# Kernel tuning notes

Hardware: AMD Instinct MI355X
Metric: run time of the kernel (lower is better)

## Reference

```python
import jax, jax.numpy as jnp
import numpy as np

EPS = 1e-8  # torch F.cosine_similarity default eps


def setup_inputs() -> dict:
    key = jax.random.key(0)
    k1, k2 = jax.random.split(key)
    xs_pad = jax.random.normal(k1, (8, 8192, 256), dtype=jnp.float32)   # [B, T, D]
    spk_emb = jax.random.normal(k2, (8, 200, 256), dtype=jnp.float32)   # [B, S, D]
    return {"xs_pad": xs_pad, "spk_emb": spk_emb}


def reference(xs_pad, spk_emb):
    # Pairwise cosine similarity: [B, T, S]
    # Equivalent to F.cosine_similarity(xs.unsqueeze(2), spk.unsqueeze(1), dim=-1)
    # = dot(x, y) / max(||x|| * ||y||, eps)
    dot = jnp.einsum("btd,bsd->bts", xs_pad, spk_emb)
    nx = jnp.linalg.norm(xs_pad, axis=-1)    # [B, T]
    ny = jnp.linalg.norm(spk_emb, axis=-1)   # [B, S]
    denom = jnp.maximum(nx[:, :, None] * ny[:, None, :], EPS)
    return dot / denom
```

## Files before the change

kernel.cpp:

```cpp
#include <hip/hip_runtime.h>
#include <math.h>

typedef __attribute__((ext_vector_type(8))) _Float16 f16x8;
typedef __attribute__((ext_vector_type(4))) float f32x4;

#define BT 8192
#define BS 200
#define SP 208
#define DD 256
#define NJ 13
#define NKB 8

#define SLOT_H 512
#define PLANE_SLOTS (8 * NKB * NJ)
#define PLANE_H ((size_t)PLANE_SLOTS * SLOT_H)
#define WS_NEED (2 * PLANE_H * 2 + 8 * SP * 4)

__global__ __launch_bounds__(256, 4)
void spk_prep_kernel(const float* __restrict__ SPK, _Float16* __restrict__ wsH) {
    const int j = blockIdx.x;
    const int b = blockIdx.y;
    const int tid = threadIdx.x;
    const int w = tid >> 6;
    const int lane = tid & 63;
    const int lr = lane & 15;
    const int lg = lane >> 4;
    const int srow = j * 16 + lr;
    const float* __restrict__ spk_b = SPK + (size_t)b * BS * DD;

    __shared__ float pn[4][16];
    float ss = 0.f;

    #pragma unroll
    for (int t = 0; t < 2; ++t) {
        int kb = w + t * 4;
        f16x8 hi, lo;
        if (srow < BS) {
            const float* src = spk_b + srow * DD + kb * 32 + lg * 8;
            float4 v0 = *(const float4*)src;
            float4 v1 = *(const float4*)(src + 4);
            float xv[8] = {v0.x, v0.y, v0.z, v0.w, v1.x, v1.y, v1.z, v1.w};
            #pragma unroll
            for (int e = 0; e < 8; ++e) {
                _Float16 h = (_Float16)xv[e];
                hi[e] = h;
                lo[e] = (_Float16)(xv[e] - (float)h);
                ss = fmaf(xv[e], xv[e], ss);
            }
        } else {
            #pragma unroll
            for (int e = 0; e < 8; ++e) { hi[e] = (_Float16)0.f; lo[e] = (_Float16)0.f; }
        }
        size_t slot = ((size_t)(b * NKB + kb) * NJ + j) * SLOT_H + lane * 8;
        *(f16x8*)&wsH[slot] = hi;
        *(f16x8*)&wsH[PLANE_H + slot] = lo;
    }

    ss += __shfl_xor(ss, 16, 64);
    ss += __shfl_xor(ss, 32, 64);
    if (lane < 16) pn[w][lane] = ss;
    __syncthreads();
    if (tid < 16) {
        float s = pn[0][tid] + pn[1][tid] + pn[2][tid] + pn[3][tid];
        float* sn = (float*)(wsH + 2 * PLANE_H);
        sn[b * SP + j * 16 + tid] = sqrtf(s);
    }
}

__global__ __launch_bounds__(256, 4)
void cos_main_kernel(const float* __restrict__ X, const _Float16* __restrict__ wsH,
                     float* __restrict__ OUT) {
    const int b   = blockIdx.y;
    const int t0  = blockIdx.x * 64;
    const int tid = threadIdx.x;
    const int wid = tid >> 6;
    const int lane = tid & 63;
    const int lr = lane & 15;
    const int lg = lane >> 4;

    const float* __restrict__ xrow = X + ((size_t)b * BT + t0 + wid * 16 + lr) * DD;
    const float* __restrict__ snW = (const float*)(wsH + 2 * PLANE_H) + b * SP;

    float4 pa0 = *(const float4*)(xrow + lg * 8);
    float4 pa1 = *(const float4*)(xrow + lg * 8 + 4);

    f32x4 acc[NJ];
    #pragma unroll
    for (int j = 0; j < NJ; ++j) acc[j] = (f32x4){0.f, 0.f, 0.f, 0.f};
    float ss = 0.f;

    for (int kb = 0; kb < NKB; ++kb) {
        f16x8 ahi, alo;
        {
            float xv[8] = {pa0.x, pa0.y, pa0.z, pa0.w, pa1.x, pa1.y, pa1.z, pa1.w};
            #pragma unroll
            for (int e = 0; e < 8; ++e) {
                _Float16 h = (_Float16)xv[e];
                ahi[e] = h;
                alo[e] = (_Float16)(xv[e] - (float)h);
                ss = fmaf(xv[e], xv[e], ss);
            }
        }
        if (kb < NKB - 1) {
            int o = (kb + 1) * 32 + lg * 8;
            pa0 = *(const float4*)(xrow + o);
            pa1 = *(const float4*)(xrow + o + 4);
        }
        const _Float16* __restrict__ base =
            wsH + ((size_t)(b * NKB + kb) * NJ) * SLOT_H + lane * 8;
        #pragma unroll
        for (int j = 0; j < NJ; ++j) {
            f16x8 bhi = *(const f16x8*)(base + (size_t)j * SLOT_H);
            f16x8 blo = *(const f16x8*)(base + PLANE_H + (size_t)j * SLOT_H);
            acc[j] = __builtin_amdgcn_mfma_f32_16x16x32_f16(ahi, bhi, acc[j], 0, 0, 0);
            acc[j] = __builtin_amdgcn_mfma_f32_16x16x32_f16(alo, bhi, acc[j], 0, 0, 0);
            acc[j] = __builtin_amdgcn_mfma_f32_16x16x32_f16(ahi, blo, acc[j], 0, 0, 0);
        }
    }

    ss += __shfl_xor(ss, 16, 64);
    ss += __shfl_xor(ss, 32, 64);

    #pragma unroll
    for (int reg = 0; reg < 4; ++reg) {
        int rc = lg * 4 + reg;
        float xn = sqrtf(__shfl(ss, rc, 64));
        int row = t0 + wid * 16 + rc;
        float* orow = OUT + ((size_t)b * BT + row) * BS;
        #pragma unroll
        for (int j = 0; j < NJ; ++j) {
            int col = j * 16 + lr;
            if (col < BS) {
                float denom = fmaxf(xn * snW[col], 1e-8f);
                orow[col] = acc[j][reg] * __builtin_amdgcn_rcpf(denom);
            }
        }
    }
}

#define TM 128
#define LSTR 40

__global__ __launch_bounds__(256, 2)
void cos_scorer_kernel(const float* __restrict__ X, const float* __restrict__ SPK,
                       float* __restrict__ OUT) {
    const int b   = blockIdx.y;
    const int t0  = blockIdx.x * TM;
    const int tid = threadIdx.x;
    const int wid = tid >> 6;
    const int lane = tid & 63;
    const int lr  = lane & 15;
    const int lg  = lane >> 4;

    __shared__ _Float16 Shi[SP * LSTR];
    __shared__ _Float16 Slo[SP * LSTR];
    __shared__ float sn_l[SP];

    const float* __restrict__ spk_b = SPK + (size_t)b * BS * DD;
    const float* __restrict__ xrow0 = X + ((size_t)b * BT + t0 + wid * 32 + lr) * DD;
    const float* __restrict__ xrow1 = xrow0 + 16 * DD;

    float4 pa00 = *(const float4*)(xrow0 + lg * 8);
    float4 pa01 = *(const float4*)(xrow0 + lg * 8 + 4);
    float4 pa10 = *(const float4*)(xrow1 + lg * 8);
    float4 pa11 = *(const float4*)(xrow1 + lg * 8 + 4);

    if (tid < SP) {
        float ss = 0.f;
        if (tid < BS) {
            const float4* p = (const float4*)(spk_b + tid * DD);
            #pragma unroll 8
            for (int i = 0; i < DD / 4; ++i) {
                float4 v = p[i];
                ss = fmaf(v.x, v.x, ss); ss = fmaf(v.y, v.y, ss);
                ss = fmaf(v.z, v.z, ss); ss = fmaf(v.w, v.w, ss);
            }
        }
        sn_l[tid] = sqrtf(ss);
    }

    f32x4 acc[2][NJ];
    #pragma unroll
    for (int rt = 0; rt < 2; ++rt)
        #pragma unroll
        for (int j = 0; j < NJ; ++j)
            acc[rt][j] = (f32x4){0.f, 0.f, 0.f, 0.f};

    float ss0 = 0.f, ss1 = 0.f;

    for (int kb = 0; kb < 8; ++kb) {
        for (int i = tid; i < SP * 4; i += 256) {
            int s = i >> 2, part = i & 3;
            f16x8 hi, lo;
            #pragma unroll
            for (int e = 0; e < 8; ++e) { hi[e] = (_Float16)0.f; lo[e] = (_Float16)0.f; }
            if (s < BS) {
                const float* src = spk_b + s * DD + kb * 32 + part * 8;
                float4 v0 = *(const float4*)src;
                float4 v1 = *(const float4*)(src + 4);
                float xv[8] = {v0.x, v0.y, v0.z, v0.w, v1.x, v1.y, v1.z, v1.w};
                #pragma unroll
                for (int e = 0; e < 8; ++e) {
                    _Float16 h = (_Float16)xv[e];
                    hi[e] = h;
                    lo[e] = (_Float16)(xv[e] - (float)h);
                }
            }
            int off = s * LSTR + part * 8;
            *(f16x8*)&Shi[off] = hi;
            *(f16x8*)&Slo[off] = lo;
        }
        __syncthreads();

        f16x8 ahi0, alo0, ahi1, alo1;
        {
            float xv0[8] = {pa00.x, pa00.y, pa00.z, pa00.w, pa01.x, pa01.y, pa01.z, pa01.w};
            float xv1[8] = {pa10.x, pa10.y, pa10.z, pa10.w, pa11.x, pa11.y, pa11.z, pa11.w};
            #pragma unroll
            for (int e = 0; e < 8; ++e) {
                _Float16 h0 = (_Float16)xv0[e];
                ahi0[e] = h0; alo0[e] = (_Float16)(xv0[e] - (float)h0);
                ss0 = fmaf(xv0[e], xv0[e], ss0);
                _Float16 h1 = (_Float16)xv1[e];
                ahi1[e] = h1; alo1[e] = (_Float16)(xv1[e] - (float)h1);
                ss1 = fmaf(xv1[e], xv1[e], ss1);
            }
        }
        if (kb < 7) {
            int o = (kb + 1) * 32 + lg * 8;
            pa00 = *(const float4*)(xrow0 + o);
            pa01 = *(const float4*)(xrow0 + o + 4);
            pa10 = *(const float4*)(xrow1 + o);
            pa11 = *(const float4*)(xrow1 + o + 4);
        }

        #pragma unroll
        for (int j = 0; j < NJ; ++j) {
            int boff = (j * 16 + lr) * LSTR + lg * 8;
            f16x8 bhi = *(const f16x8*)&Shi[boff];
            f16x8 blo = *(const f16x8*)&Slo[boff];
            acc[0][j] = __builtin_amdgcn_mfma_f32_16x16x32_f16(ahi0, bhi, acc[0][j], 0, 0, 0);
            acc[1][j] = __builtin_amdgcn_mfma_f32_16x16x32_f16(ahi1, bhi, acc[1][j], 0, 0, 0);
            acc[0][j] = __builtin_amdgcn_mfma_f32_16x16x32_f16(alo0, bhi, acc[0][j], 0, 0, 0);
            acc[1][j] = __builtin_amdgcn_mfma_f32_16x16x32_f16(alo1, bhi, acc[1][j], 0, 0, 0);
            acc[0][j] = __builtin_amdgcn_mfma_f32_16x16x32_f16(ahi0, blo, acc[0][j], 0, 0, 0);
            acc[1][j] = __builtin_amdgcn_mfma_f32_16x16x32_f16(ahi1, blo, acc[1][j], 0, 0, 0);
        }
        __syncthreads();
    }

    ss0 += __shfl_xor(ss0, 16, 64);
    ss0 += __shfl_xor(ss0, 32, 64);
    ss1 += __shfl_xor(ss1, 16, 64);
    ss1 += __shfl_xor(ss1, 32, 64);

    #pragma unroll
    for (int rt = 0; rt < 2; ++rt) {
        float ssv = rt ? ss1 : ss0;
        #pragma unroll
        for (int reg = 0; reg < 4; ++reg) {
            int rc = lg * 4 + reg;
            float xn = sqrtf(__shfl(ssv, rc, 64));
            int row = t0 + wid * 32 + rt * 16 + rc;
            float* orow = OUT + ((size_t)b * BT + row) * BS;
            #pragma unroll
            for (int j = 0; j < NJ; ++j) {
                int col = j * 16 + lr;
                if (col < BS) {
                    float denom = fmaxf(xn * sn_l[col], 1e-8f);
                    orow[col] = acc[rt][j][reg] * __builtin_amdgcn_rcpf(denom);
                }
            }
        }
    }
}

extern "C" void kernel_launch(void* const* d_in, const int* in_sizes, int n_in,
                              void* d_out, int out_size, void* d_ws, size_t ws_size,
                              hipStream_t stream) {
    const float* X   = (const float*)d_in[0];
    const float* SPK = (const float*)d_in[1];
    float* OUT = (float*)d_out;

    if (ws_size >= (size_t)WS_NEED) {
        _Float16* wsH = (_Float16*)d_ws;
        hipLaunchKernelGGL(spk_prep_kernel, dim3(NJ, 8), dim3(256), 0, stream, SPK, wsH);
        hipLaunchKernelGGL(cos_main_kernel, dim3(BT / 64, 8), dim3(256), 0, stream,
                           X, wsH, OUT);
    } else {
        hipLaunchKernelGGL(cos_scorer_kernel, dim3(BT / TM, 8), dim3(256), 0, stream,
                           X, SPK, OUT);
    }
}
```

Before: 147.7 us.

## Stage speaker fragments in double-buffered LDS and give each wave two row tiles

The main kernel now copies the prepped fp16 hi/lo speaker fragments into a double-buffered shared-memory tile with direct global-to-LDS loads, prefetching the next k-block while the MFMAs run on the current one. Each wave handles two 16-row tiles instead of one, so every B fragment read from LDS feeds twice as many MFMAs. The workspace layout interleaves the hi and lo planes per k-block to make each copy contiguous. In exchange the kernel needs more accumulator registers (launch bounds 4 to 2), a block barrier per k-step, and half as many blocks.

```diff
diff --git a/kernel.cpp b/kernel.cpp
--- a/kernel.cpp
+++ b/kernel.cpp
@@ -10,11 +10,17 @@
 #define DD 256
 #define NJ 13
 #define NKB 8
-
+#define NSLOT 26
 #define SLOT_H 512
-#define PLANE_SLOTS (8 * NKB * NJ)
-#define PLANE_H ((size_t)PLANE_SLOTS * SLOT_H)
-#define WS_NEED (2 * PLANE_H * 2 + 8 * SP * 4)
+#define TOT_SLOTS (8 * NKB * NSLOT)
+#define NORM_OFF ((size_t)TOT_SLOTS * SLOT_H)
+#define WS_NEED (NORM_OFF * 2 + 8 * SP * 4)
+
+__device__ __forceinline__ void gl_lds16(const _Float16* g, _Float16* l) {
+    __builtin_amdgcn_global_load_lds(
+        (const __attribute__((address_space(1))) unsigned int*)g,
+        (__attribute__((address_space(3))) unsigned int*)l, 16, 0, 0);
+}
 
 __global__ __launch_bounds__(256, 4)
 void spk_prep_kernel(const float* __restrict__ SPK, _Float16* __restrict__ wsH) {
@@ -51,9 +57,9 @@
             #pragma unroll
             for (int e = 0; e < 8; ++e) { hi[e] = (_Float16)0.f; lo[e] = (_Float16)0.f; }
         }
-        size_t slot = ((size_t)(b * NKB + kb) * NJ + j) * SLOT_H + lane * 8;
-        *(f16x8*)&wsH[slot] = hi;
-        *(f16x8*)&wsH[PLANE_H + slot] = lo;
+        size_t base = ((size_t)(b * NKB + kb) * NSLOT + j) * SLOT_H + lane * 8;
+        *(f16x8*)&wsH[base] = hi;
+        *(f16x8*)&wsH[base + 13 * SLOT_H] = lo;
     }
 
     ss += __shfl_xor(ss, 16, 64);
@@ -62,77 +68,117 @@
     __syncthreads();
     if (tid < 16) {
         float s = pn[0][tid] + pn[1][tid] + pn[2][tid] + pn[3][tid];
-        float* sn = (float*)(wsH + 2 * PLANE_H);
+        float* sn = (float*)(wsH + NORM_OFF);
         sn[b * SP + j * 16 + tid] = sqrtf(s);
     }
 }
 
-__global__ __launch_bounds__(256, 4)
+__global__ __launch_bounds__(256, 2)
 void cos_main_kernel(const float* __restrict__ X, const _Float16* __restrict__ wsH,
                      float* __restrict__ OUT) {
     const int b   = blockIdx.y;
-    const int t0  = blockIdx.x * 64;
+    const int t0  = blockIdx.x * 128;
     const int tid = threadIdx.x;
     const int wid = tid >> 6;
     const int lane = tid & 63;
     const int lr = lane & 15;
     const int lg = lane >> 4;
 
-    const float* __restrict__ xrow = X + ((size_t)b * BT + t0 + wid * 16 + lr) * DD;
-    const float* __restrict__ snW = (const float*)(wsH + 2 * PLANE_H) + b * SP;
-
-    float4 pa0 = *(const float4*)(xrow + lg * 8);
-    float4 pa1 = *(const float4*)(xrow + lg * 8 + 4);
-
-    f32x4 acc[NJ];
-    #pragma unroll
-    for (int j = 0; j < NJ; ++j) acc[j] = (f32x4){0.f, 0.f, 0.f, 0.f};
-    float ss = 0.f;
+    __shared__ _Float16 Bb[2][NSLOT * SLOT_H];
+
+    const float* __restrict__ xrow0 = X + ((size_t)b * BT + t0 + wid * 32 + lr) * DD;
+    const float* __restrict__ xrow1 = xrow0 + 16 * DD;
+    const float* __restrict__ snW = (const float*)(wsH + NORM_OFF) + b * SP;
+    const _Float16* __restrict__ wsB = wsH + (size_t)b * NKB * NSLOT * SLOT_H;
+
+    float4 pa00 = *(const float4*)(xrow0 + lg * 8);
+    float4 pa01 = *(const float4*)(xrow0 + lg * 8 + 4);
+    float4 pa10 = *(const float4*)(xrow1 + lg * 8);
+    float4 pa11 = *(const float4*)(xrow1 + lg * 8 + 4);
+
+    for (int s = wid; s < NSLOT; s += 4)
+        gl_lds16(wsB + (size_t)s * SLOT_H + lane * 8, &Bb[0][s * SLOT_H]);
+    __syncthreads();
+
+    f32x4 acc[2][NJ];
+    #pragma unroll
+    for (int rt = 0; rt < 2; ++rt)
+        #pragma unroll
+        for (int j = 0; j < NJ; ++j)
+            acc[rt][j] = (f32x4){0.f, 0.f, 0.f, 0.f};
+
+    float ss0 = 0.f, ss1 = 0.f;
+    int cur = 0;
 
     for (int kb = 0; kb < NKB; ++kb) {
-        f16x8 ahi, alo;
+        if (kb < NKB - 1) {
+            const _Float16* src = wsB + (size_t)(kb + 1) * NSLOT * SLOT_H;
+            for (int s = wid; s < NSLOT; s += 4)
+                gl_lds16(src + (size_t)s * SLOT_H + lane * 8, &Bb[cur ^ 1][s * SLOT_H]);
+        }
+
+        f16x8 ahi0, alo0, ahi1, alo1;
         {
-            float xv[8] = {pa0.x, pa0.y, pa0.z, pa0.w, pa1.x, pa1.y, pa1.z, pa1.w};
+            float xv0[8] = {pa00.x, pa00.y, pa00.z, pa00.w, pa01.x, pa01.y, pa01.z, pa01.w};
+            float xv1[8] = {pa10.x, pa10.y, pa10.z, pa10.w, pa11.x, pa11.y, pa11.z, pa11.w};
             #pragma unroll
             for (int e = 0; e < 8; ++e) {
-                _Float16 h = (_Float16)xv[e];
-                ahi[e] = h;
-                alo[e] = (_Float16)(xv[e] - (float)h);
-                ss = fmaf(xv[e], xv[e], ss);
+                _Float16 h0 = (_Float16)xv0[e];
+                ahi0[e] = h0; alo0[e] = (_Float16)(xv0[e] - (float)h0);
+                ss0 = fmaf(xv0[e], xv0[e], ss0);
+                _Float16 h1 = (_Float16)xv1[e];
+                ahi1[e] = h1; alo1[e] = (_Float16)(xv1[e] - (float)h1);
+                ss1 = fmaf(xv1[e], xv1[e], ss1);
             }
         }
         if (kb < NKB - 1) {
             int o = (kb + 1) * 32 + lg * 8;
-            pa0 = *(const float4*)(xrow + o);
-            pa1 = *(const float4*)(xrow + o + 4);
-        }
-        const _Float16* __restrict__ base =
-            wsH + ((size_t)(b * NKB + kb) * NJ) * SLOT_H + lane * 8;
+            pa00 = *(const float4*)(xrow0 + o);
+            pa01 = *(const float4*)(xrow0 + o + 4);
+            pa10 = *(const float4*)(xrow1 + o);
+            pa11 = *(const float4*)(xrow1 + o + 4);
+        }
+
+        const _Float16* __restrict__ bc = &Bb[cur][lane * 8];
         #pragma unroll
         for (int j = 0; j < NJ; ++j) {
-            f16x8 bhi = *(const f16x8*)(base + (size_t)j * SLOT_H);
-            f16x8 blo = *(const f16x8*)(base + PLANE_H + (size_t)j * SLOT_H);
-            acc[j] = __builtin_amdgcn_mfma_f32_16x16x32_f16(ahi, bhi, acc[j], 0, 0, 0);
-            acc[j] = __builtin_amdgcn_mfma_f32_16x16x32_f16(alo, bhi, acc[j], 0, 0, 0);
-            acc[j] = __builtin_amdgcn_mfma_f32_16x16x32_f16(ahi, blo, acc[j], 0, 0, 0);
-        }
-    }
-
-    ss += __shfl_xor(ss, 16, 64);
-    ss += __shfl_xor(ss, 32, 64);
-
-    #pragma unroll
-    for (int reg = 0; reg < 4; ++reg) {
-        int rc = lg * 4 + reg;
-        float xn = sqrtf(__shfl(ss, rc, 64));
-        int row = t0 + wid * 16 + rc;
-        float* orow = OUT + ((size_t)b * BT + row) * BS;
-        #pragma unroll
-        for (int j = 0; j < NJ; ++j) {
-            int col = j * 16 + lr;
-            if (col < BS) {
-                float denom = fmaxf(xn * snW[col], 1e-8f);
-                orow[col] = acc[j][reg] * __builtin_amdgcn_rcpf(denom);
+            f16x8 bhi = *(const f16x8*)(bc + j * SLOT_H);
+            f16x8 blo = *(const f16x8*)(bc + (13 + j) * SLOT_H);
+            acc[0][j] = __builtin_amdgcn_mfma_f32_16x16x32_f16(ahi0, bhi, acc[0][j], 0, 0, 0);
+            acc[1][j] = __builtin_amdgcn_mfma_f32_16x16x32_f16(ahi1, bhi, acc[1][j], 0, 0, 0);
+            acc[0][j] = __builtin_amdgcn_mfma_f32_16x16x32_f16(alo0, bhi, acc[0][j], 0, 0, 0);
+            acc[1][j] = __builtin_amdgcn_mfma_f32_16x16x32_f16(alo1, bhi, acc[1][j], 0, 0, 0);
+            acc[0][j] = __builtin_amdgcn_mfma_f32_16x16x32_f16(ahi0, blo, acc[0][j], 0, 0, 0);
+            acc[1][j] = __builtin_amdgcn_mfma_f32_16x16x32_f16(ahi1, blo, acc[1][j], 0, 0, 0);
+        }
+
+        if (kb < NKB - 1) {
+            __syncthreads();
+            cur ^= 1;
+        }
+    }
+
+    ss0 += __shfl_xor(ss0, 16, 64);
+    ss0 += __shfl_xor(ss0, 32, 64);
+    ss1 += __shfl_xor(ss1, 16, 64);
+    ss1 += __shfl_xor(ss1, 32, 64);
+
+    #pragma unroll
+    for (int rt = 0; rt < 2; ++rt) {
+        float ssv = rt ? ss1 : ss0;
+        #pragma unroll
+        for (int reg = 0; reg < 4; ++reg) {
+            int rc = lg * 4 + reg;
+            float xn = sqrtf(__shfl(ssv, rc, 64));
+            int row = t0 + wid * 32 + rt * 16 + rc;
+            float* orow = OUT + ((size_t)b * BT + row) * BS;
+            #pragma unroll
+            for (int j = 0; j < NJ; ++j) {
+                int col = j * 16 + lr;
+                if (col < BS) {
+                    float denom = fmaxf(xn * snW[col], 1e-8f);
+                    orow[col] = acc[rt][j][reg] * __builtin_amdgcn_rcpf(denom);
+                }
             }
         }
     }
@@ -285,7 +331,7 @@
     if (ws_size >= (size_t)WS_NEED) {
         _Float16* wsH = (_Float16*)d_ws;
         hipLaunchKernelGGL(spk_prep_kernel, dim3(NJ, 8), dim3(256), 0, stream, SPK, wsH);
-        hipLaunchKernelGGL(cos_main_kernel, dim3(BT / 64, 8), dim3(256), 0, stream,
+        hipLaunchKernelGGL(cos_main_kernel, dim3(BT / 128, 8), dim3(256), 0, stream,
                            X, wsH, OUT);
     } else {
         hipLaunchKernelGGL(cos_scorer_kernel, dim3(BT / TM, 8), dim3(256), 0, stream,
```

Result: faster. 122.4 us (-17.1%).

## Stage speaker fp16 tiles in LDS with double-buffered async loads

Applied to the files above, without the earlier changes.

Interleaves the hi/lo speaker planes per k-block in the workspace so each k-block is one contiguous 26-slot chunk. The main kernel now uses 512-thread blocks covering 128 rows and stages that chunk into double-buffered LDS with global_load_lds, so the next k-block's load overlaps the current MFMAs. It also raises wave priority around the MFMA groups. This replaces per-wave redundant global B loads with shared LDS reuse, at the cost of LDS use, a barrier per k-block, and a hand-written vmcnt wait that may be wrong because the X prefetch loads also count toward vmcnt.

```diff
diff --git a/kernel.cpp b/kernel.cpp
--- a/kernel.cpp
+++ b/kernel.cpp
@@ -10,11 +10,17 @@
 #define DD 256
 #define NJ 13
 #define NKB 8
-
+#define NSLOT 26
 #define SLOT_H 512
-#define PLANE_SLOTS (8 * NKB * NJ)
-#define PLANE_H ((size_t)PLANE_SLOTS * SLOT_H)
-#define WS_NEED (2 * PLANE_H * 2 + 8 * SP * 4)
+#define TOT_SLOTS (8 * NKB * NSLOT)
+#define NORM_OFF ((size_t)TOT_SLOTS * SLOT_H)
+#define WS_NEED (NORM_OFF * 2 + 8 * SP * 4)
+
+__device__ __forceinline__ void gl_lds16(const _Float16* g, _Float16* l) {
+    __builtin_amdgcn_global_load_lds(
+        (const __attribute__((address_space(1))) unsigned int*)g,
+        (__attribute__((address_space(3))) unsigned int*)l, 16, 0, 0);
+}
 
 __global__ __launch_bounds__(256, 4)
 void spk_prep_kernel(const float* __restrict__ SPK, _Float16* __restrict__ wsH) {
@@ -51,9 +57,9 @@
             #pragma unroll
             for (int e = 0; e < 8; ++e) { hi[e] = (_Float16)0.f; lo[e] = (_Float16)0.f; }
         }
-        size_t slot = ((size_t)(b * NKB + kb) * NJ + j) * SLOT_H + lane * 8;
-        *(f16x8*)&wsH[slot] = hi;
-        *(f16x8*)&wsH[PLANE_H + slot] = lo;
+        size_t base = ((size_t)(b * NKB + kb) * NSLOT + j) * SLOT_H + lane * 8;
+        *(f16x8*)&wsH[base] = hi;
+        *(f16x8*)&wsH[base + 13 * SLOT_H] = lo;
     }
 
     ss += __shfl_xor(ss, 16, 64);
@@ -62,34 +68,50 @@
     __syncthreads();
     if (tid < 16) {
         float s = pn[0][tid] + pn[1][tid] + pn[2][tid] + pn[3][tid];
-        float* sn = (float*)(wsH + 2 * PLANE_H);
+        float* sn = (float*)(wsH + NORM_OFF);
         sn[b * SP + j * 16 + tid] = sqrtf(s);
     }
 }
 
-__global__ __launch_bounds__(256, 4)
+__global__ __launch_bounds__(512, 4)
 void cos_main_kernel(const float* __restrict__ X, const _Float16* __restrict__ wsH,
                      float* __restrict__ OUT) {
     const int b   = blockIdx.y;
-    const int t0  = blockIdx.x * 64;
+    const int t0  = blockIdx.x * 128;
     const int tid = threadIdx.x;
     const int wid = tid >> 6;
     const int lane = tid & 63;
     const int lr = lane & 15;
     const int lg = lane >> 4;
 
+    __shared__ _Float16 Bb[2][NSLOT * SLOT_H];
+
     const float* __restrict__ xrow = X + ((size_t)b * BT + t0 + wid * 16 + lr) * DD;
-    const float* __restrict__ snW = (const float*)(wsH + 2 * PLANE_H) + b * SP;
+    const float* __restrict__ snW = (const float*)(wsH + NORM_OFF) + b * SP;
+    const _Float16* __restrict__ wsB = wsH + (size_t)b * NKB * NSLOT * SLOT_H;
 
     float4 pa0 = *(const float4*)(xrow + lg * 8);
     float4 pa1 = *(const float4*)(xrow + lg * 8 + 4);
 
+    for (int s = wid; s < NSLOT; s += 8)
+        gl_lds16(wsB + (size_t)s * SLOT_H + lane * 8, &Bb[0][s * SLOT_H]);
+    __syncthreads();
+
     f32x4 acc[NJ];
     #pragma unroll
     for (int j = 0; j < NJ; ++j) acc[j] = (f32x4){0.f, 0.f, 0.f, 0.f};
+
     float ss = 0.f;
+    int cur = 0;
 
     for (int kb = 0; kb < NKB; ++kb) {
+        if (kb < NKB - 1) {
+            const _Float16* src = wsB + (size_t)(kb + 1) * NSLOT * SLOT_H;
+            for (int s = wid; s < NSLOT; s += 8)
+                gl_lds16(src + (size_t)s * SLOT_H + lane * 8, &Bb[cur ^ 1][s * SLOT_H]);
+            __builtin_amdgcn_sched_barrier(0);
+        }
+
         f16x8 ahi, alo;
         {
             float xv[8] = {pa0.x, pa0.y, pa0.z, pa0.w, pa1.x, pa1.y, pa1.z, pa1.w};
@@ -106,15 +128,24 @@
             pa0 = *(const float4*)(xrow + o);
             pa1 = *(const float4*)(xrow + o + 4);
         }
-        const _Float16* __restrict__ base =
-            wsH + ((size_t)(b * NKB + kb) * NJ) * SLOT_H + lane * 8;
+
+        const _Float16* __restrict__ bc = &Bb[cur][lane * 8];
         #pragma unroll
         for (int j = 0; j < NJ; ++j) {
-            f16x8 bhi = *(const f16x8*)(base + (size_t)j * SLOT_H);
-            f16x8 blo = *(const f16x8*)(base + PLANE_H + (size_t)j * SLOT_H);
+            f16x8 bhi = *(const f16x8*)(bc + j * SLOT_H);
+            f16x8 blo = *(const f16x8*)(bc + (13 + j) * SLOT_H);
+            __builtin_amdgcn_s_setprio(1);
             acc[j] = __builtin_amdgcn_mfma_f32_16x16x32_f16(ahi, bhi, acc[j], 0, 0, 0);
             acc[j] = __builtin_amdgcn_mfma_f32_16x16x32_f16(alo, bhi, acc[j], 0, 0, 0);
             acc[j] = __builtin_amdgcn_mfma_f32_16x16x32_f16(ahi, blo, acc[j], 0, 0, 0);
+            __builtin_amdgcn_s_setprio(0);
+        }
+
+        if (kb < NKB - 1) {
+            asm volatile("s_waitcnt vmcnt(2)" ::: "memory");
+            __builtin_amdgcn_s_barrier();
+            __builtin_amdgcn_sched_barrier(0);
+            cur ^= 1;
         }
     }
 
@@ -285,7 +316,7 @@
     if (ws_size >= (size_t)WS_NEED) {
         _Float16* wsH = (_Float16*)d_ws;
         hipLaunchKernelGGL(spk_prep_kernel, dim3(NJ, 8), dim3(256), 0, stream, SPK, wsH);
-        hipLaunchKernelGGL(cos_main_kernel, dim3(BT / 64, 8), dim3(256), 0, stream,
+        hipLaunchKernelGGL(cos_main_kernel, dim3(BT / 128, 8), dim3(512), 0, stream,
                            X, wsH, OUT);
     } else {
         hipLaunchKernelGGL(cos_scorer_kernel, dim3(BT / TM, 8), dim3(256), 0, stream,
```

New measurement: 123.3 us. 1.2x faster.
